# Optimization experiments

Measured on AMD Instinct MI355X. Metric: run time of the kernel, lower is better.

## Reference

```python
import jax, jax.numpy as jnp
import numpy as np
import math

D_MODEL = 1024
HEAD_DIM = 256
GAMMA = 0.9


def setup_inputs() -> dict:
    key = jax.random.key(0)
    k1, k2, k3, k4 = jax.random.split(key, 4)
    B, L = 4, 4096
    x = jax.random.normal(k1, (B, L, D_MODEL), dtype=jnp.float32)
    s = 1.0 / math.sqrt(D_MODEL)
    W_Q = jax.random.normal(k2, (HEAD_DIM, D_MODEL), dtype=jnp.float32) * s
    W_K = jax.random.normal(k3, (HEAD_DIM, D_MODEL), dtype=jnp.float32) * s
    W_V = jax.random.normal(k4, (HEAD_DIM, D_MODEL), dtype=jnp.float32) * s
    return {"x": x, "W_Q": W_Q, "W_K": W_K, "W_V": W_V}


def _decay_mask(L: int, gamma: float) -> jnp.ndarray:
    # D[i,j] = gamma^(i-j) if i >= j else 0
    idx = jnp.arange(L)
    diff = idx[:, None] - idx[None, :]
    return jnp.where(diff >= 0, jnp.power(jnp.float32(gamma), diff.astype(jnp.float32)), 0.0)


def reference(x, W_Q, W_K, W_V):
    B, L, _ = x.shape
    Q = jnp.einsum('bld,hd->blh', x, W_Q)  # (B,L,H)
    K = jnp.einsum('bld,hd->blh', x, W_K)
    V = jnp.einsum('bld,hd->blh', x, W_V)
    D = _decay_mask(L, GAMMA)  # (L,L)
    scores = jnp.einsum('bih,bjh->bij', Q, K) * D[None, :, :]
    scores = scores / jnp.sqrt(jnp.float32(HEAD_DIM))
    return jnp.einsum('bij,bjh->bih', scores, V)  # (B,L,H)
```

## Files before the change

kernel.cpp:

```cpp
#include <hip/hip_runtime.h>

typedef unsigned short u16;
typedef unsigned int u32;
typedef __attribute__((ext_vector_type(8))) short bf16x8;
typedef __attribute__((ext_vector_type(4))) float f32x4;
typedef __attribute__((ext_vector_type(4))) unsigned short u16x4;

#define DEVI __device__ __forceinline__

constexpr float L2GAMMA = -0.15200309344504997f;
constexpr float INV_SQRT_H = 0.0625f;

DEVI u16 f2bf(float x) {
  union { float f; unsigned u; } v; v.f = x;
  unsigned r = v.u + 0x7FFFu + ((v.u >> 16) & 1u);
  return (u16)(r >> 16);
}

DEVI u32 pack2bf(float f0, float f1) {
  u32 u0 = __float_as_uint(f0) + 0x8000u;
  u32 u1 = __float_as_uint(f1) + 0x8000u;
  return __builtin_amdgcn_perm(u1, u0, 0x07060302u);
}

__global__ void cvt_w_kernel(const float4* __restrict__ wq, const float4* __restrict__ wk,
                             const float4* __restrict__ wv, u16x4* __restrict__ dst) {
  int i = blockIdx.x * blockDim.x + threadIdx.x;
  int w = i >> 16, off = i & 65535;
  const float4* s = (w == 0) ? wq : ((w == 1) ? wk : wv);
  float4 v = s[off];
  u16x4 o; o.x = f2bf(v.x); o.y = f2bf(v.y); o.z = f2bf(v.z); o.w = f2bf(v.w);
  dst[(w << 16) + off] = o;
}

__global__ __launch_bounds__(512, 2) void qkv_gemm_kernel(const float* __restrict__ Xf, const u16* __restrict__ Wb,
                                                          u16* __restrict__ Qb, u16* __restrict__ Kb,
                                                          u16* __restrict__ Vt) {
  __shared__ u16 Blds[3][24576];
  __shared__ u16 Alds[2][2048];
  const int bid = blockIdx.x;
  const int m0 = bid << 6;
  const int tid = threadIdx.x;
  const int wid = tid >> 6, lane = tid & 63;
  const int lrow = lane & 15, lkg = lane >> 4;
  const int brow = lane >> 2;
  const int bcol = ((lane & 3) ^ ((lane >> 3) & 3)) << 3;
  const int arow = tid >> 3, af4 = tid & 7;
  const float* aload = Xf + (size_t)(m0 + arow) * 1024 + af4 * 4;
  const int awr = arow * 32 + ((((af4 >> 1) ^ ((arow >> 1) & 3)) << 3) | ((af4 & 1) << 2));
  const int sw = (lkg ^ ((lrow >> 1) & 3)) << 3;

#define BSTAGE(T, WB) do { \
  _Pragma("unroll") for (int j_ = 0; j_ < 6; ++j_) { \
    const int c_ = wid * 6 + j_; \
    const u16* g_ = Wb + (size_t)(c_ * 16 + brow) * 1024 + (T) * 32 + bcol; \
    __builtin_amdgcn_global_load_lds((const __attribute__((address_space(1))) void*)g_, \
        (__attribute__((address_space(3))) void*)&Blds[WB][c_ * 512], 16, 0, 0); } } while (0)

#define ALOAD(T, REG) do { REG = *(const float4*)(aload + (size_t)(T) * 32); } while (0)

#define ACVT(REG, AB) do { \
  uint2 pk_; pk_.x = pack2bf(REG.x, REG.y); pk_.y = pack2bf(REG.z, REG.w); \
  *(uint2*)&Alds[AB][awr] = pk_; } while (0)

#define COMPUTE(RB, AB) do { \
  const u16* Ab_ = Alds[AB]; const u16* Bb_ = Blds[RB]; \
  bf16x8 af_[4], bf_[6]; \
  _Pragma("unroll") for (int mf = 0; mf < 4; ++mf) \
    af_[mf] = *(const bf16x8*)&Ab_[(mf * 16 + lrow) * 32 + sw]; \
  _Pragma("unroll") for (int nf = 0; nf < 6; ++nf) \
    bf_[nf] = *(const bf16x8*)&Bb_[(wid * 96 + nf * 16 + lrow) * 32 + sw]; \
  __builtin_amdgcn_s_setprio(1); \
  _Pragma("unroll") for (int mf = 0; mf < 4; ++mf) \
    _Pragma("unroll") for (int nf = 0; nf < 6; ++nf) \
      acc[mf][nf] = __builtin_amdgcn_mfma_f32_16x16x32_bf16(af_[mf], bf_[nf], acc[mf][nf], 0, 0, 0); \
  __builtin_amdgcn_s_setprio(0); } while (0)

  f32x4 acc[4][6] = {};
  float4 aS0, aS1;

  ALOAD(0, aS0); ALOAD(1, aS1);
  BSTAGE(0, 0); BSTAGE(1, 1);
  ACVT(aS0, 0);
  asm volatile("s_waitcnt vmcnt(7)" ::: "memory");
  asm volatile("s_waitcnt lgkmcnt(0)" ::: "memory");
  __builtin_amdgcn_s_barrier();

  int rb = 0, wb = 2;
  for (int ti = 0; ti < 16; ++ti) {
    const bool pf = ti < 15;
    if (pf) { ALOAD(2 * ti + 2, aS0); BSTAGE(2 * ti + 2, wb); }
    __builtin_amdgcn_sched_barrier(0);
    COMPUTE(rb, 0);
    __builtin_amdgcn_sched_barrier(0);
    ACVT(aS1, 1);
    if (pf) { asm volatile("s_waitcnt vmcnt(7)" ::: "memory"); }
    else    { asm volatile("s_waitcnt vmcnt(0)" ::: "memory"); }
    asm volatile("s_waitcnt lgkmcnt(0)" ::: "memory");
    __builtin_amdgcn_s_barrier();
    rb = (rb == 2) ? 0 : rb + 1; wb = (wb == 2) ? 0 : wb + 1;
    if (pf) { ALOAD(2 * ti + 3, aS1); BSTAGE(2 * ti + 3, wb); }
    __builtin_amdgcn_sched_barrier(0);
    COMPUTE(rb, 1);
    __builtin_amdgcn_sched_barrier(0);
    if (pf) {
      ACVT(aS0, 0);
      asm volatile("s_waitcnt vmcnt(7)" ::: "memory");
      asm volatile("s_waitcnt lgkmcnt(0)" ::: "memory");
      __builtin_amdgcn_s_barrier();
    }
    rb = (rb == 2) ? 0 : rb + 1; wb = (wb == 2) ? 0 : wb + 1;
  }

#pragma unroll
  for (int mf = 0; mf < 4; ++mf)
#pragma unroll
    for (int nf = 0; nf < 6; ++nf) {
      const int gm = m0 + mf * 16 + lkg * 4;
      const int c = wid * 96 + nf * 16 + lrow;
      if (c < 512) {
        u16* Dst = (c < 256) ? Qb : Kb;
        const int cc = c & 255;
#pragma unroll
        for (int r = 0; r < 4; ++r) Dst[(size_t)(gm + r) * 256 + cc] = f2bf(acc[mf][nf][r]);
      } else {
        const int h = c - 512;
        const int bb = gm >> 12, l = gm & 4095;
        u16x4 pk;
        pk.x = f2bf(acc[mf][nf][0]); pk.y = f2bf(acc[mf][nf][1]);
        pk.z = f2bf(acc[mf][nf][2]); pk.w = f2bf(acc[mf][nf][3]);
        *(u16x4*)&Vt[((size_t)bb * 256 + h) * 4096 + l] = pk;
      }
    }
}

__global__ __launch_bounds__(256) void attn_kernel(const u16* __restrict__ Qb, const u16* __restrict__ Kb,
                                                   const u16* __restrict__ Vt, float* __restrict__ out) {
  __shared__ u16 Plds[32 * 72];
  const int raw = blockIdx.x;
  const int aid = (raw & 7) * 64 + (raw >> 3);
  const int b = aid >> 7;
  const int qt = aid & 127;
  const int qb = qt * 32;
  const int tid = threadIdx.x;
  const int wid = tid >> 6, lane = tid & 63;
  const int lrow = lane & 15, lkg = lane >> 4, lk = lkg * 8;
  const size_t bQK = (size_t)b * 4096 * 256;

  bf16x8 qf[2][8];
#pragma unroll
  for (int mf = 0; mf < 2; ++mf) {
    const u16* Qrow = Qb + bQK + (size_t)(qb + mf * 16 + lrow) * 256;
#pragma unroll
    for (int kf = 0; kf < 8; ++kf) qf[mf][kf] = *(const bf16x8*)&Qrow[kf * 32 + lk];
  }

  int kstart = qb - 256; if (kstart < 0) kstart = 0; kstart &= ~63;
  const int njt = (qb + 32 - kstart + 63) >> 6;

  f32x4 oacc[2][4] = {};

  for (int jt = 0; jt < njt; ++jt) {
    const int kb = kstart + jt * 64;
    f32x4 s[2] = {};
    const u16* Krow = Kb + bQK + (size_t)(kb + wid * 16 + lrow) * 256;
#pragma unroll
    for (int kf = 0; kf < 8; ++kf) {
      const bf16x8 kfr = *(const bf16x8*)&Krow[kf * 32 + lk];
      s[0] = __builtin_amdgcn_mfma_f32_16x16x32_bf16(qf[0][kf], kfr, s[0], 0, 0, 0);
      s[1] = __builtin_amdgcn_mfma_f32_16x16x32_bf16(qf[1][kf], kfr, s[1], 0, 0, 0);
    }
    const int kg = kb + wid * 16 + lrow;
#pragma unroll
    for (int mf = 0; mf < 2; ++mf) {
      const int qg = qb + mf * 16 + lkg * 4;
#pragma unroll
      for (int r = 0; r < 4; ++r) {
        const int d = qg + r - kg;
        const float pv = (d >= 0) ? s[mf][r] * exp2f((float)d * L2GAMMA) * INV_SQRT_H : 0.0f;
        Plds[(mf * 16 + lkg * 4 + r) * 72 + wid * 16 + lrow] = f2bf(pv);
      }
    }
    __syncthreads();
#pragma unroll
    for (int ks = 0; ks < 2; ++ks) {
      bf16x8 pa[2];
      pa[0] = *(const bf16x8*)&Plds[(lrow) * 72 + ks * 32 + lk];
      pa[1] = *(const bf16x8*)&Plds[(16 + lrow) * 72 + ks * 32 + lk];
#pragma unroll
      for (int nf = 0; nf < 4; ++nf) {
        const bf16x8 vb = *(const bf16x8*)&Vt[((size_t)b * 256 + wid * 64 + nf * 16 + lrow) * 4096 + kb + ks * 32 + lk];
        oacc[0][nf] = __builtin_amdgcn_mfma_f32_16x16x32_bf16(pa[0], vb, oacc[0][nf], 0, 0, 0);
        oacc[1][nf] = __builtin_amdgcn_mfma_f32_16x16x32_bf16(pa[1], vb, oacc[1][nf], 0, 0, 0);
      }
    }
    __syncthreads();
  }

#pragma unroll
  for (int mf = 0; mf < 2; ++mf) {
    float* obase = out + ((size_t)b * 4096 + qb + mf * 16 + lkg * 4) * 256 + wid * 64 + lrow;
#pragma unroll
    for (int nf = 0; nf < 4; ++nf)
#pragma unroll
      for (int r = 0; r < 4; ++r)
        obase[(size_t)r * 256 + nf * 16] = oacc[mf][nf][r];
  }
}

extern "C" void kernel_launch(void* const* d_in, const int* in_sizes, int n_in,
                              void* d_out, int out_size, void* d_ws, size_t ws_size,
                              hipStream_t stream) {
  const float* x  = (const float*)d_in[0];
  const float* wq = (const float*)d_in[1];
  const float* wk = (const float*)d_in[2];
  const float* wv = (const float*)d_in[3];
  float* out = (float*)d_out;
  char* ws = (char*)d_ws;
  u16* Wb = (u16*)(ws);
  u16* Qb = (u16*)(ws + (size_t)1572864);
  u16* Kb = (u16*)(ws + (size_t)9961472);
  u16* Vt = (u16*)(ws + (size_t)18350080);

  hipLaunchKernelGGL(cvt_w_kernel, dim3(768), dim3(256), 0, stream,
                     (const float4*)wq, (const float4*)wk, (const float4*)wv, (u16x4*)Wb);
  hipLaunchKernelGGL(qkv_gemm_kernel, dim3(256), dim3(512), 0, stream, x, Wb, Qb, Kb, Vt);
  hipLaunchKernelGGL(attn_kernel, dim3(512), dim3(256), 0, stream, Qb, Kb, Vt, out);
}
```

Before: 89.76 us.

## Retile QKV GEMM to 256x192 blocks with K-step 64 and XCD-aware mapping

Changes the QKV projection GEMM from 64-row blocks that each cover all 768 output columns to 256x192 tiles. It also doubles the K step to 64, uses a 2x4 wave layout, and adds an XCD-aware block-to-tile mapping so blocks sharing X rows land on the same XCD. The aim is better operand reuse per LDS load and less redundant W traffic across blocks, since the old layout reloaded all of W for every 64-row block. In exchange X is now read four times, once per column tile, and each thread holds more registers and LDS. The extra pressure could limit occupancy, and the pipeline depth is reduced.

Measured after the change: 79.42 us. -11.5%, faster.

```diff
diff --git a/kernel.cpp b/kernel.cpp
--- a/kernel.cpp
+++ b/kernel.cpp
@@ -7,6 +7,8 @@
 typedef __attribute__((ext_vector_type(4))) unsigned short u16x4;
 
 #define DEVI __device__ __forceinline__
+#define AS1 __attribute__((address_space(1)))
+#define AS3 __attribute__((address_space(3)))
 
 constexpr float L2GAMMA = -0.15200309344504997f;
 constexpr float INV_SQRT_H = 0.0625f;
@@ -36,88 +38,81 @@
 __global__ __launch_bounds__(512, 2) void qkv_gemm_kernel(const float* __restrict__ Xf, const u16* __restrict__ Wb,
                                                           u16* __restrict__ Qb, u16* __restrict__ Kb,
                                                           u16* __restrict__ Vt) {
-  __shared__ u16 Blds[3][24576];
-  __shared__ u16 Alds[2][2048];
+  __shared__ u16 Al[2][256 * 64];
+  __shared__ u16 Bl[3][192 * 64];
   const int bid = blockIdx.x;
-  const int m0 = bid << 6;
+  const int xcd = bid & 7, seq = bid >> 3;
+  const int m0 = (xcd * 8 + (seq >> 2)) * 256;
+  const int n0 = (seq & 3) * 192;
   const int tid = threadIdx.x;
   const int wid = tid >> 6, lane = tid & 63;
+  const int wm = wid >> 2, wn = wid & 3;
   const int lrow = lane & 15, lkg = lane >> 4;
-  const int brow = lane >> 2;
-  const int bcol = ((lane & 3) ^ ((lane >> 3) & 3)) << 3;
-  const int arow = tid >> 3, af4 = tid & 7;
-  const float* aload = Xf + (size_t)(m0 + arow) * 1024 + af4 * 4;
-  const int awr = arow * 32 + ((((af4 >> 1) ^ ((arow >> 1) & 3)) << 3) | ((af4 & 1) << 2));
-  const int sw = (lkg ^ ((lrow >> 1) & 3)) << 3;
-
-#define BSTAGE(T, WB) do { \
-  _Pragma("unroll") for (int j_ = 0; j_ < 6; ++j_) { \
-    const int c_ = wid * 6 + j_; \
-    const u16* g_ = Wb + (size_t)(c_ * 16 + brow) * 1024 + (T) * 32 + bcol; \
-    __builtin_amdgcn_global_load_lds((const __attribute__((address_space(1))) void*)g_, \
-        (__attribute__((address_space(3))) void*)&Blds[WB][c_ * 512], 16, 0, 0); } } while (0)
-
-#define ALOAD(T, REG) do { REG = *(const float4*)(aload + (size_t)(T) * 32); } while (0)
-
-#define ACVT(REG, AB) do { \
-  uint2 pk_; pk_.x = pack2bf(REG.x, REG.y); pk_.y = pack2bf(REG.z, REG.w); \
-  *(uint2*)&Alds[AB][awr] = pk_; } while (0)
-
-#define COMPUTE(RB, AB) do { \
-  const u16* Ab_ = Alds[AB]; const u16* Bb_ = Blds[RB]; \
-  bf16x8 af_[4], bf_[6]; \
-  _Pragma("unroll") for (int mf = 0; mf < 4; ++mf) \
-    af_[mf] = *(const bf16x8*)&Ab_[(mf * 16 + lrow) * 32 + sw]; \
-  _Pragma("unroll") for (int nf = 0; nf < 6; ++nf) \
-    bf_[nf] = *(const bf16x8*)&Bb_[(wid * 96 + nf * 16 + lrow) * 32 + sw]; \
+
+  const int a_r = tid >> 4, a_s = tid & 15;
+  const float* a_g = Xf + (size_t)(m0 + a_r) * 1024 + a_s * 4;
+  const int a_wr = a_r * 64 + (((a_s >> 1) ^ (a_r & 7)) << 3) + ((a_s & 1) << 2);
+  const int b_r = tid >> 3;
+  const u16* b_g = Wb + (size_t)(n0 + b_r) * 1024 + (((tid & 7) ^ (b_r & 7)) << 3);
+
+  float4 ar[8];
+
+#define ALOAD(T) do { const float* g_ = a_g + (T) * 64; \
+  _Pragma("unroll") for (int j_ = 0; j_ < 8; ++j_) \
+    ar[j_] = *(const float4*)(g_ + (size_t)j_ * 32 * 1024); } while (0)
+
+#define ACVT(P) do { \
+  _Pragma("unroll") for (int j_ = 0; j_ < 8; ++j_) { \
+    uint2 pk_; pk_.x = pack2bf(ar[j_].x, ar[j_].y); pk_.y = pack2bf(ar[j_].z, ar[j_].w); \
+    *(uint2*)&Al[P][j_ * 2048 + a_wr] = pk_; } } while (0)
+
+#define BSTAGE(T, BUF) do { const u16* g_ = b_g + (T) * 64; \
+  _Pragma("unroll") for (int j_ = 0; j_ < 3; ++j_) \
+    __builtin_amdgcn_global_load_lds((const AS1 void*)(g_ + (size_t)j_ * 64 * 1024), \
+        (AS3 void*)&Bl[BUF][j_ * 4096 + tid * 8], 16, 0, 0); } while (0)
+
+#define KKSTEP(KK, P, BQ) do { bf16x8 af_[8], bf_[3]; \
+  const int ps_ = (((KK) * 4 + lkg) ^ (lrow & 7)) << 3; \
+  _Pragma("unroll") for (int mf = 0; mf < 8; ++mf) \
+    af_[mf] = *(const bf16x8*)&Al[P][(wm * 128 + mf * 16 + lrow) * 64 + ps_]; \
+  _Pragma("unroll") for (int nf = 0; nf < 3; ++nf) \
+    bf_[nf] = *(const bf16x8*)&Bl[BQ][(wn * 48 + nf * 16 + lrow) * 64 + ps_]; \
   __builtin_amdgcn_s_setprio(1); \
-  _Pragma("unroll") for (int mf = 0; mf < 4; ++mf) \
-    _Pragma("unroll") for (int nf = 0; nf < 6; ++nf) \
+  _Pragma("unroll") for (int mf = 0; mf < 8; ++mf) \
+    _Pragma("unroll") for (int nf = 0; nf < 3; ++nf) \
       acc[mf][nf] = __builtin_amdgcn_mfma_f32_16x16x32_bf16(af_[mf], bf_[nf], acc[mf][nf], 0, 0, 0); \
   __builtin_amdgcn_s_setprio(0); } while (0)
 
-  f32x4 acc[4][6] = {};
-  float4 aS0, aS1;
-
-  ALOAD(0, aS0); ALOAD(1, aS1);
+  f32x4 acc[8][3] = {};
+
+  ALOAD(0);
   BSTAGE(0, 0); BSTAGE(1, 1);
-  ACVT(aS0, 0);
-  asm volatile("s_waitcnt vmcnt(7)" ::: "memory");
-  asm volatile("s_waitcnt lgkmcnt(0)" ::: "memory");
+  ACVT(0);
+  asm volatile("s_waitcnt vmcnt(3) lgkmcnt(0)" ::: "memory");
   __builtin_amdgcn_s_barrier();
 
-  int rb = 0, wb = 2;
-  for (int ti = 0; ti < 16; ++ti) {
-    const bool pf = ti < 15;
-    if (pf) { ALOAD(2 * ti + 2, aS0); BSTAGE(2 * ti + 2, wb); }
-    __builtin_amdgcn_sched_barrier(0);
-    COMPUTE(rb, 0);
-    __builtin_amdgcn_sched_barrier(0);
-    ACVT(aS1, 1);
-    if (pf) { asm volatile("s_waitcnt vmcnt(7)" ::: "memory"); }
-    else    { asm volatile("s_waitcnt vmcnt(0)" ::: "memory"); }
-    asm volatile("s_waitcnt lgkmcnt(0)" ::: "memory");
-    __builtin_amdgcn_s_barrier();
-    rb = (rb == 2) ? 0 : rb + 1; wb = (wb == 2) ? 0 : wb + 1;
-    if (pf) { ALOAD(2 * ti + 3, aS1); BSTAGE(2 * ti + 3, wb); }
-    __builtin_amdgcn_sched_barrier(0);
-    COMPUTE(rb, 1);
-    __builtin_amdgcn_sched_barrier(0);
-    if (pf) {
-      ACVT(aS0, 0);
-      asm volatile("s_waitcnt vmcnt(7)" ::: "memory");
-      asm volatile("s_waitcnt lgkmcnt(0)" ::: "memory");
+  int p = 0, bq = 0, wq = 2;
+  for (int t = 0; t < 16; ++t) {
+    if (t + 1 < 16) ALOAD(t + 1);
+    if (t + 2 < 16) BSTAGE(t + 2, wq);
+    KKSTEP(0, p, bq);
+    if (t + 1 < 16) ACVT(p ^ 1);
+    KKSTEP(1, p, bq);
+    if (t < 15) {
+      asm volatile("s_waitcnt vmcnt(3) lgkmcnt(0)" ::: "memory");
       __builtin_amdgcn_s_barrier();
     }
-    rb = (rb == 2) ? 0 : rb + 1; wb = (wb == 2) ? 0 : wb + 1;
-  }
-
-#pragma unroll
-  for (int mf = 0; mf < 4; ++mf)
-#pragma unroll
-    for (int nf = 0; nf < 6; ++nf) {
-      const int gm = m0 + mf * 16 + lkg * 4;
-      const int c = wid * 96 + nf * 16 + lrow;
+    p ^= 1;
+    bq = (bq == 2) ? 0 : bq + 1;
+    wq = (wq == 2) ? 0 : wq + 1;
+  }
+
+#pragma unroll
+  for (int mf = 0; mf < 8; ++mf)
+#pragma unroll
+    for (int nf = 0; nf < 3; ++nf) {
+      const int gm = m0 + wm * 128 + mf * 16 + lkg * 4;
+      const int c = n0 + wn * 48 + nf * 16 + lrow;
       if (c < 512) {
         u16* Dst = (c < 256) ? Qb : Kb;
         const int cc = c & 255;
```
